# Kernel tuning notes

Measured on AMD Instinct MI355X. Metric: run time of the kernel, lower is better.

The kernel has to match this reference:

```python
import jax, jax.numpy as jnp
import numpy as np

EMBED_DIM = 1024
NUM_HEADS = 16
HEAD_WIDTH = 64  # EMBED_DIM == NUM_HEADS * HEAD_WIDTH
B, L = 2, 1024


def setup_inputs() -> dict:
    key = jax.random.key(0)
    ks = jax.random.split(key, 7)
    s = EMBED_DIM ** -0.5
    return {
        "x": jax.random.normal(ks[0], (B, L, EMBED_DIM), dtype=jnp.float32),
        "bias": jax.random.normal(ks[1], (B, L, L, NUM_HEADS), dtype=jnp.float32),
        # nn.Linear weights are (out_features, in_features)
        "w_proj": jax.random.normal(ks[2], (3 * EMBED_DIM, EMBED_DIM), dtype=jnp.float32) * s,
        "w_o": jax.random.normal(ks[3], (EMBED_DIM, EMBED_DIM), dtype=jnp.float32) * s,
        "b_o": jnp.zeros((EMBED_DIM,), dtype=jnp.float32),
        "w_g": jax.random.normal(ks[4], (EMBED_DIM, EMBED_DIM), dtype=jnp.float32) * s,
        "b_g": jnp.ones((EMBED_DIM,), dtype=jnp.float32),
    }


def reference(x, bias, w_proj, w_o, b_o, w_g, b_g):
    b, l, e = x.shape
    h, hw = NUM_HEADS, HEAD_WIDTH
    # fused QKV projection: (B,L,3E) -> (B,H,L,3*hw), head-major split as in torch
    t = jnp.einsum('ble,fe->blf', x, w_proj)
    t = t.reshape(b, l, h, 3 * hw).transpose(0, 2, 1, 3)  # (B,H,L,3hw)
    q, k, v = jnp.split(t, 3, axis=-1)
    q = q * (hw ** -0.5)
    a = jnp.einsum('bhqc,bhkc->bhqk', q, k)
    a = a + bias.transpose(0, 3, 1, 2)  # bias: (B,Lq,Lk,H) -> (B,H,Lq,Lk)
    a = jax.nn.softmax(a, axis=-1)
    y = jnp.einsum('bhqk,bhkc->bqhc', a, v).reshape(b, l, e)
    g = jax.nn.sigmoid(jnp.einsum('ble,fe->blf', x, w_g) + b_g)
    y = g * y
    y = jnp.einsum('ble,fe->blf', y, w_o) + b_o
    # faithful to original rearrange('... lq lk h -> ... h lq lk') applied to (B,h,lq,lk):
    attn = jnp.transpose(a, (0, 3, 1, 2))  # (B, lk, h, lq)
    return y, attn
```

## Files before the change

kernel.cpp:

```cpp
#include <hip/hip_runtime.h>
#include <hip/hip_bf16.h>
#include <stdint.h>

typedef __attribute__((ext_vector_type(4))) float f32x4;
typedef __attribute__((ext_vector_type(8))) short short8;
typedef __attribute__((ext_vector_type(4))) unsigned short u16x4;
typedef unsigned short us;

#define DEV __device__ __forceinline__
#define MFMA16(a, b, c) __builtin_amdgcn_mfma_f32_16x16x32_bf16(a, b, c, 0, 0, 0)

DEV us f2b(float x) {
  union { float f; uint32_t u; } c; c.f = x;
  uint32_t r = (c.u + 0x7fffu + ((c.u >> 16) & 1u)) >> 16;
  return (us)r;
}
DEV float b2f(us x) {
  union { uint32_t u; float f; } c; c.u = ((uint32_t)x) << 16;
  return c.f;
}

DEV void gload_lds16(const void* g, void* l) {
  __builtin_amdgcn_global_load_lds((const __attribute__((address_space(1))) void*)g,
                                   (__attribute__((address_space(3))) void*)l, 16, 0, 0);
}

__global__ __launch_bounds__(256) void prep_k(
    const float* __restrict__ x, const float* __restrict__ wproj,
    const float* __restrict__ wg, const float* __restrict__ wo,
    us* __restrict__ Xbf, us* __restrict__ Wbf, us* __restrict__ Wobf) {
  int i = blockIdx.x * 256 + threadIdx.x;
  const float* src; us* dst;
  if (i < 524288)               { src = x     + (size_t)i * 4;                  dst = Xbf + (size_t)i * 4; }
  else if (i < 524288 + 786432) { int j = i - 524288;            src = wproj + (size_t)j * 4; dst = Wbf + (size_t)j * 4; }
  else if (i < 524288 + 786432 + 262144) { int j = i - (524288 + 786432); src = wg + (size_t)j * 4; dst = Wbf + 3145728 + (size_t)j * 4; }
  else                          { int j = i - (524288 + 786432 + 262144); src = wo + (size_t)j * 4; dst = Wobf + (size_t)j * 4; }
  f32x4 v = *(const f32x4*)src;
  u16x4 o; o.x = f2b(v.x); o.y = f2b(v.y); o.z = f2b(v.z); o.w = f2b(v.w);
  *(u16x4*)dst = o;
}

DEV void gemm_stage(char* sm, const us* A, const us* Bw,
                    int tileMrow, int tileNrow, int buf, int kt, int lane, int wid) {
  const char* gA = (const char*)A;
  const char* gB = (const char*)Bw;
#pragma unroll
  for (int i = 0; i < 2; ++i) {
    int c = wid * 2 + i;
    int off = c * 1024 + lane * 16;
    int r = off >> 6, cb = off & 63;
    gload_lds16(gA + ((size_t)(tileMrow + r) * 2048) + kt * 64 + cb, sm + buf * 8192 + c * 1024);
    gload_lds16(gB + ((size_t)(tileNrow + r) * 2048) + kt * 64 + cb, sm + 16384 + buf * 8192 + c * 1024);
  }
}

DEV void gemm_main(const us* A, const us* Bw,
                   int tileMrow, int tileNrow, f32x4 acc[4][4], char* sm) {
  int tid = threadIdx.x, lane = tid & 63, wid = tid >> 6;
  int wr = wid >> 1, wc = wid & 1;
  gemm_stage(sm, A, Bw, tileMrow, tileNrow, 0, 0, lane, wid);
  for (int kt = 0; kt < 32; ++kt) {
    __syncthreads();
    if (kt < 31) gemm_stage(sm, A, Bw, tileMrow, tileNrow, (kt + 1) & 1, kt + 1, lane, wid);
    int ab = (kt & 1) * 8192;
    int rb = (lane & 15) * 64 + ((lane >> 4) * 16);
    short8 af[4], bf[4];
#pragma unroll
    for (int mi = 0; mi < 4; ++mi)
      af[mi] = *(const short8*)(sm + ab + (wr * 64 + mi * 16) * 64 + rb);
#pragma unroll
    for (int ni = 0; ni < 4; ++ni)
      bf[ni] = *(const short8*)(sm + 16384 + ab + (wc * 64 + ni * 16) * 64 + rb);
#pragma unroll
    for (int mi = 0; mi < 4; ++mi)
#pragma unroll
      for (int ni = 0; ni < 4; ++ni)
        acc[mi][ni] = MFMA16(af[mi], bf[ni], acc[mi][ni]);
  }
}

__global__ __launch_bounds__(256) void gemm_qkvg_k(
    const us* __restrict__ Xbf, const us* __restrict__ Wbf,
    us* __restrict__ Qb, us* __restrict__ Kb, us* __restrict__ Vt,
    float* __restrict__ G, const float* __restrict__ bg) {
  __shared__ char sm[32768];
  int bid = blockIdx.x;
  int swz = (bid & 7) * 64 + (bid >> 3);
  int tileM = swz >> 5, tileN = swz & 31;
  f32x4 acc[4][4] = {};
  gemm_main(Xbf, Wbf, tileM * 128, tileN * 128, acc, sm);
  int lane = threadIdx.x & 63, wid = threadIdx.x >> 6;
  int wr = wid >> 1, wc = wid & 1;
#pragma unroll
  for (int mi = 0; mi < 4; ++mi)
#pragma unroll
    for (int ni = 0; ni < 4; ++ni)
#pragma unroll
      for (int j = 0; j < 4; ++j) {
        int row = tileM * 128 + wr * 64 + mi * 16 + ((lane >> 4) << 2) + j;
        int col = tileN * 128 + wc * 64 + ni * 16 + (lane & 15);
        float v = acc[mi][ni][j];
        int b = row >> 10, l = row & 1023;
        if (col < 3072) {
          int h = col / 192, r = col - h * 192;
          size_t base = ((size_t)(b * 16 + h) * 1024 + l) * 64;
          if (r < 64)        Qb[base + r] = f2b(v * 0.125f);
          else if (r < 128)  Kb[base + (r - 64)] = f2b(v);
          else               Vt[((size_t)(b * 16 + h) * 64 + (r - 128)) * 1024 + l] = f2b(v);
        } else {
          int e = col - 3072;
          float s = v + bg[e];
          G[(size_t)row * 1024 + e] = 1.f / (1.f + __expf(-s));
        }
      }
}

__global__ __launch_bounds__(512, 4) void qke_k(
    const us* __restrict__ Qb, const us* __restrict__ Kb,
    const float* __restrict__ bias, us* __restrict__ E,
    float* __restrict__ lpart) {
  __shared__ float bt[2][4][8][16][36];
  int tid = threadIdx.x, lane = tid & 63, w = tid >> 6;
  int la = lane & 15, lg = lane >> 4;
  int bid = blockIdx.x;
  int b = (bid & 7) >> 2, kc = bid & 3;
  int hg = (bid >> 3) & 1, qt = bid >> 4;
  int lq0 = qt * 16, lk00 = kc * 256;
  int h = hg * 8 + w, hh = w;

  short8 qf[2];
  {
    size_t bh = (size_t)(b * 16 + h);
#pragma unroll
    for (int ks = 0; ks < 2; ++ks)
      qf[ks] = *(const short8*)(Qb + bh * 65536 + (size_t)(lq0 + la) * 64 + ks * 32 + lg * 8);
  }
  const us* Kh = Kb + (size_t)(b * 16 + h) * 65536;
  const float* bsrc = bias + ((size_t)b << 24) + ((size_t)lq0 << 14) + hg * 8;
  us* Erow = E + (((size_t)(b * 1024 + lq0 + la) * 16 + h) << 10);

  f32x4 vv[8];
#pragma unroll
  for (int i = 0; i < 8; ++i) {
    int f = i * 512 + tid;
    int h4 = f & 1, lk = (f >> 1) & 127, q = f >> 8;
    vv[i] = *(const f32x4*)(bsrc + ((size_t)q << 14) + ((size_t)(lk00 + lk) << 4) + h4 * 4);
  }
#pragma unroll
  for (int i = 0; i < 8; ++i) {
    int f = i * 512 + tid;
    int h4 = f & 1, lk = (f >> 1) & 127, q = f >> 8;
    int c = lk >> 5, slk = lk & 31;
#pragma unroll
    for (int e = 0; e < 4; ++e) {
      int hl = h4 * 4 + e;
      bt[0][c][hl][q][slk ^ (hl << 2)] = vv[i][e];
    }
  }
  __syncthreads();

  float lacc = 0.f;
#pragma unroll
  for (int i = 0; i < 8; ++i) {
    int f = i * 512 + tid;
    int h4 = f & 1, lk = (f >> 1) & 127, q = f >> 8;
    vv[i] = *(const f32x4*)(bsrc + ((size_t)q << 14) + ((size_t)(lk00 + 128 + lk) << 4) + h4 * 4);
  }
#pragma unroll
  for (int fr = 0; fr < 8; ++fr) {
    int c = fr >> 1;
    const us* kr = Kh + (size_t)(lk00 + fr * 16 + la) * 64 + lg * 8;
    short8 kf0 = *(const short8*)kr;
    short8 kf1 = *(const short8*)(kr + 32);
    int lkb = ((fr & 1) * 16 + lg * 4) ^ (hh << 2);
    f32x4 a = *(const f32x4*)&bt[0][c][hh][la][lkb];
    a = MFMA16(kf0, qf[0], a);
    a = MFMA16(kf1, qf[1], a);
    u16x4 ev;
#pragma unroll
    for (int j = 0; j < 4; ++j) {
      float e = __expf(a[j]);
      lacc += e;
      ev[j] = f2b(e);
    }
    *(u16x4*)(Erow + lk00 + fr * 16 + lg * 4) = ev;
  }
#pragma unroll
  for (int i = 0; i < 8; ++i) {
    int f = i * 512 + tid;
    int h4 = f & 1, lk = (f >> 1) & 127, q = f >> 8;
    int c = lk >> 5, slk = lk & 31;
#pragma unroll
    for (int e = 0; e < 4; ++e) {
      int hl = h4 * 4 + e;
      bt[1][c][hl][q][slk ^ (hl << 2)] = vv[i][e];
    }
  }
  __syncthreads();
#pragma unroll
  for (int fr = 0; fr < 8; ++fr) {
    int c = fr >> 1;
    const us* kr = Kh + (size_t)(lk00 + 128 + fr * 16 + la) * 64 + lg * 8;
    short8 kf0 = *(const short8*)kr;
    short8 kf1 = *(const short8*)(kr + 32);
    int lkb = ((fr & 1) * 16 + lg * 4) ^ (hh << 2);
    f32x4 a = *(const f32x4*)&bt[1][c][hh][la][lkb];
    a = MFMA16(kf0, qf[0], a);
    a = MFMA16(kf1, qf[1], a);
    u16x4 ev;
#pragma unroll
    for (int j = 0; j < 4; ++j) {
      float e = __expf(a[j]);
      lacc += e;
      ev[j] = f2b(e);
    }
    *(u16x4*)(Erow + lk00 + 128 + fr * 16 + lg * 4) = ev;
  }
  {
    float s = lacc;
    s += __shfl_xor(s, 16);
    s += __shfl_xor(s, 32);
    if (lg == 0) lpart[kc * 32768 + (b * 16 + h) * 1024 + lq0 + la] = s;
  }
}

__global__ __launch_bounds__(256) void pv_k(
    const us* __restrict__ E, const us* __restrict__ Vt,
    const float* __restrict__ lpart, const float* __restrict__ G,
    float* __restrict__ outa, us* __restrict__ Ybf) {
  __shared__ char sm[49792];
  float* lv = (float*)(sm + 49664);
  int tid = threadIdx.x, lane = tid & 63, w = tid >> 6;
  int la = lane & 15, lg = lane >> 4;
  int bid = blockIdx.x;
  int g = bid >> 8, qt = (bid >> 3) & 31, xx = bid & 7;
  int bh = g * 8 + xx;
  int b = bh >> 4, h = bh & 15;
  int qb = qt * 32;
  if (tid < 32) {
    int r = bh * 1024 + qb + tid;
    float s = lpart[r] + lpart[32768 + r] + lpart[65536 + r] + lpart[98304 + r];
    lv[tid] = 1.f / s;
  }
  __syncthreads();
  char* pb = sm + w * 4096;
  const us* Vh = Vt + (size_t)bh * 65536;
  f32x4 yacc[2][4] = {};
  int lkw = w * 256;

#pragma unroll 1
  for (int cc = 0; cc < 4; ++cc) {
    int lk0 = lkw + cc * 64;
#pragma unroll
    for (int it = 0; it < 4; ++it) {
      int ci = it * 64 + lane;
      int q = ci >> 3, c16 = ci & 7;
      short8 ev = *(const short8*)(E + (((size_t)(b * 1024 + qb + q) * 16 + h) << 10) + lk0 + c16 * 8);
      *(short8*)(pb + q * 128 + ((c16 * 16) ^ ((q & 7) << 4))) = ev;
    }
#pragma unroll
    for (int it = 0; it < 8; ++it) {
      int idx = it * 64 + lane;
      int lkL = idx >> 3, q4 = idx & 7;
      f32x4 ov;
#pragma unroll
      for (int i = 0; i < 4; ++i) {
        int q = q4 * 4 + i;
        us e = *(const us*)(pb + q * 128 + ((2 * lkL) ^ ((q & 7) << 4)));
        ov[i] = b2f(e) * lv[q];
      }
      *(f32x4*)(outa + (((size_t)(b * 1024 + lk0 + lkL) * 16 + h) << 10) + qb + q4 * 4) = ov;
    }
#pragma unroll
    for (int ks = 0; ks < 2; ++ks) {
      short8 pa[2];
#pragma unroll
      for (int qh = 0; qh < 2; ++qh) {
        int row = qh * 16 + la;
        pa[qh] = *(const short8*)(pb + row * 128 + ((ks * 64 + lg * 16) ^ ((row & 7) << 4)));
      }
#pragma unroll
      for (int ni = 0; ni < 4; ++ni) {
        short8 vf = *(const short8*)(Vh + (size_t)(ni * 16 + la) * 1024 + lk0 + ks * 32 + lg * 8);
        yacc[0][ni] = MFMA16(pa[0], vf, yacc[0][ni]);
        yacc[1][ni] = MFMA16(pa[1], vf, yacc[1][ni]);
      }
    }
  }

  float* red = (float*)(sm + 16384);
#pragma unroll
  for (int qh = 0; qh < 2; ++qh)
#pragma unroll
    for (int ni = 0; ni < 4; ++ni)
#pragma unroll
      for (int j = 0; j < 4; ++j) {
        int r = qh * 16 + lg * 4 + j, c = ni * 16 + la;
        red[w * 2080 + r * 65 + c] = yacc[qh][ni][j];
      }
  __syncthreads();
#pragma unroll
  for (int rr = 0; rr < 8; ++rr) {
    int e = rr * 256 + tid;
    int r = e >> 6, c = e & 63;
    float s = red[r * 65 + c] + red[2080 + r * 65 + c] +
              red[4160 + r * 65 + c] + red[6240 + r * 65 + c];
    size_t gi = (((size_t)(b * 1024 + qb + r)) << 10) + h * 64 + c;
    Ybf[gi] = f2b(s * lv[r] * G[gi]);
  }
}

__global__ __launch_bounds__(256) void gemm_out_k(
    const us* __restrict__ Ybf, const us* __restrict__ Wobf,
    const float* __restrict__ bo, float* __restrict__ outy) {
  __shared__ char sm[32768];
  int bid = blockIdx.x;
  int swz = (bid & 7) * 16 + (bid >> 3);
  int tileM = swz >> 3, tileN = swz & 7;
  f32x4 acc[4][4] = {};
  gemm_main(Ybf, Wobf, tileM * 128, tileN * 128, acc, sm);
  int lane = threadIdx.x & 63, wid = threadIdx.x >> 6;
  int wr = wid >> 1, wc = wid & 1;
#pragma unroll
  for (int mi = 0; mi < 4; ++mi)
#pragma unroll
    for (int ni = 0; ni < 4; ++ni)
#pragma unroll
      for (int j = 0; j < 4; ++j) {
        int row = tileM * 128 + wr * 64 + mi * 16 + ((lane >> 4) << 2) + j;
        int col = tileN * 128 + wc * 64 + ni * 16 + (lane & 15);
        outy[(size_t)row * 1024 + col] = acc[mi][ni][j] + bo[col];
      }
}

extern "C" void kernel_launch(void* const* d_in, const int* in_sizes, int n_in,
                              void* d_out, int out_size, void* d_ws, size_t ws_size,
                              hipStream_t stream) {
  const float* x     = (const float*)d_in[0];
  const float* bias  = (const float*)d_in[1];
  const float* wproj = (const float*)d_in[2];
  const float* wo    = (const float*)d_in[3];
  const float* bo    = (const float*)d_in[4];
  const float* wg    = (const float*)d_in[5];
  const float* bg    = (const float*)d_in[6];
  float* outy = (float*)d_out;
  float* outa = outy + 2097152;

  char* ws = (char*)d_ws;
  us*    Xbf  = (us*)(ws);
  us*    Wbf  = (us*)(ws + 4  * 1024 * 1024);
  us*    Wobf = (us*)(ws + 12 * 1024 * 1024);
  us*    Qb   = (us*)(ws + 14 * 1024 * 1024);
  us*    Kb   = (us*)(ws + 18 * 1024 * 1024);
  us*    Vt   = (us*)(ws + 22 * 1024 * 1024);
  float* G    = (float*)(ws + 26 * 1024 * 1024);
  us*    Ybf  = (us*)(ws + 34 * 1024 * 1024);
  float* lpart= (float*)(ws + (size_t)38 * 1024 * 1024);
  us*    E    = (us*)   (ws + (size_t)40 * 1024 * 1024);
  if (ws_size < (size_t)104 * 1024 * 1024) return;

  prep_k<<<dim3(7168), dim3(256), 0, stream>>>(x, wproj, wg, wo, Xbf, Wbf, Wobf);
  gemm_qkvg_k<<<dim3(512), dim3(256), 0, stream>>>(Xbf, Wbf, Qb, Kb, Vt, G, bg);
  qke_k<<<dim3(1024), dim3(512), 0, stream>>>(Qb, Kb, bias, E, lpart);
  pv_k<<<dim3(1024), dim3(256), 0, stream>>>(E, Vt, lpart, G, outa, Ybf);
  gemm_out_k<<<dim3(128), dim3(256), 0, stream>>>(Ybf, Wobf, bo, outy);
}
```

Baseline: 195.1 us.

## Restructure qke kernel to cover all heads per block with 4-stage bias pipeline

Each qke block now covers all 16 heads, with each wave handling two heads, instead of splitting heads across two blocks. Bias reads therefore fetch full 64-byte head rows per key position, giving more contiguous global loads. The key range is processed in four 64-wide chunks with a double-buffered LDS prefetch loop, and the grid is halved. This trades per-block parallelism and occupancy (launch bound min-blocks removed, more registers for two Q fragments) for better bias coalescing and deeper overlap.

```diff
diff --git a/kernel.cpp b/kernel.cpp
--- a/kernel.cpp
+++ b/kernel.cpp
@@ -115,112 +115,108 @@
       }
 }
 
-__global__ __launch_bounds__(512, 4) void qke_k(
+__global__ __launch_bounds__(512) void qke_k(
     const us* __restrict__ Qb, const us* __restrict__ Kb,
     const float* __restrict__ bias, us* __restrict__ E,
     float* __restrict__ lpart) {
-  __shared__ float bt[2][4][8][16][36];
+  __shared__ float bt[2][2][16][16][36];
   int tid = threadIdx.x, lane = tid & 63, w = tid >> 6;
   int la = lane & 15, lg = lane >> 4;
   int bid = blockIdx.x;
   int b = (bid & 7) >> 2, kc = bid & 3;
-  int hg = (bid >> 3) & 1, qt = bid >> 4;
+  int qt = bid >> 3;
   int lq0 = qt * 16, lk00 = kc * 256;
-  int h = hg * 8 + w, hh = w;
-
-  short8 qf[2];
-  {
-    size_t bh = (size_t)(b * 16 + h);
+
+  short8 qf[2][2];
+#pragma unroll
+  for (int s = 0; s < 2; ++s) {
+    size_t bh = (size_t)(b * 16 + w * 2 + s);
 #pragma unroll
     for (int ks = 0; ks < 2; ++ks)
-      qf[ks] = *(const short8*)(Qb + bh * 65536 + (size_t)(lq0 + la) * 64 + ks * 32 + lg * 8);
-  }
-  const us* Kh = Kb + (size_t)(b * 16 + h) * 65536;
-  const float* bsrc = bias + ((size_t)b << 24) + ((size_t)lq0 << 14) + hg * 8;
-  us* Erow = E + (((size_t)(b * 1024 + lq0 + la) * 16 + h) << 10);
+      qf[s][ks] = *(const short8*)(Qb + bh * 65536 + (size_t)(lq0 + la) * 64 + ks * 32 + lg * 8);
+  }
+  const float* bsrc = bias + ((size_t)b << 24) + ((size_t)lq0 << 14);
 
   f32x4 vv[8];
 #pragma unroll
   for (int i = 0; i < 8; ++i) {
     int f = i * 512 + tid;
-    int h4 = f & 1, lk = (f >> 1) & 127, q = f >> 8;
+    int h4 = f & 3, lk = (f >> 2) & 63, q = f >> 8;
     vv[i] = *(const f32x4*)(bsrc + ((size_t)q << 14) + ((size_t)(lk00 + lk) << 4) + h4 * 4);
   }
 #pragma unroll
   for (int i = 0; i < 8; ++i) {
     int f = i * 512 + tid;
-    int h4 = f & 1, lk = (f >> 1) & 127, q = f >> 8;
+    int h4 = f & 3, lk = (f >> 2) & 63, q = f >> 8;
     int c = lk >> 5, slk = lk & 31;
 #pragma unroll
     for (int e = 0; e < 4; ++e) {
-      int hl = h4 * 4 + e;
-      bt[0][c][hl][q][slk ^ (hl << 2)] = vv[i][e];
-    }
-  }
-  __syncthreads();
-
-  float lacc = 0.f;
-#pragma unroll
-  for (int i = 0; i < 8; ++i) {
-    int f = i * 512 + tid;
-    int h4 = f & 1, lk = (f >> 1) & 127, q = f >> 8;
-    vv[i] = *(const f32x4*)(bsrc + ((size_t)q << 14) + ((size_t)(lk00 + 128 + lk) << 4) + h4 * 4);
-  }
-#pragma unroll
-  for (int fr = 0; fr < 8; ++fr) {
-    int c = fr >> 1;
-    const us* kr = Kh + (size_t)(lk00 + fr * 16 + la) * 64 + lg * 8;
-    short8 kf0 = *(const short8*)kr;
-    short8 kf1 = *(const short8*)(kr + 32);
-    int lkb = ((fr & 1) * 16 + lg * 4) ^ (hh << 2);
-    f32x4 a = *(const f32x4*)&bt[0][c][hh][la][lkb];
-    a = MFMA16(kf0, qf[0], a);
-    a = MFMA16(kf1, qf[1], a);
-    u16x4 ev;
-#pragma unroll
-    for (int j = 0; j < 4; ++j) {
-      float e = __expf(a[j]);
-      lacc += e;
-      ev[j] = f2b(e);
-    }
-    *(u16x4*)(Erow + lk00 + fr * 16 + lg * 4) = ev;
-  }
-#pragma unroll
-  for (int i = 0; i < 8; ++i) {
-    int f = i * 512 + tid;
-    int h4 = f & 1, lk = (f >> 1) & 127, q = f >> 8;
-    int c = lk >> 5, slk = lk & 31;
-#pragma unroll
-    for (int e = 0; e < 4; ++e) {
-      int hl = h4 * 4 + e;
-      bt[1][c][hl][q][slk ^ (hl << 2)] = vv[i][e];
-    }
-  }
-  __syncthreads();
-#pragma unroll
-  for (int fr = 0; fr < 8; ++fr) {
-    int c = fr >> 1;
-    const us* kr = Kh + (size_t)(lk00 + 128 + fr * 16 + la) * 64 + lg * 8;
-    short8 kf0 = *(const short8*)kr;
-    short8 kf1 = *(const short8*)(kr + 32);
-    int lkb = ((fr & 1) * 16 + lg * 4) ^ (hh << 2);
-    f32x4 a = *(const f32x4*)&bt[1][c][hh][la][lkb];
-    a = MFMA16(kf0, qf[0], a);
-    a = MFMA16(kf1, qf[1], a);
-    u16x4 ev;
-#pragma unroll
-    for (int j = 0; j < 4; ++j) {
-      float e = __expf(a[j]);
-      lacc += e;
-      ev[j] = f2b(e);
-    }
-    *(u16x4*)(Erow + lk00 + 128 + fr * 16 + lg * 4) = ev;
-  }
-  {
-    float s = lacc;
-    s += __shfl_xor(s, 16);
-    s += __shfl_xor(s, 32);
-    if (lg == 0) lpart[kc * 32768 + (b * 16 + h) * 1024 + lq0 + la] = s;
+      int h = h4 * 4 + e;
+      bt[0][c][h][q][slk ^ ((h & 7) << 2)] = vv[i][e];
+    }
+  }
+
+  float lacc[2] = {0.f, 0.f};
+#pragma unroll 1
+  for (int t = 0; t < 4; ++t) {
+    __syncthreads();
+    if (t < 3) {
+      int lkt = lk00 + (t + 1) * 64;
+#pragma unroll
+      for (int i = 0; i < 8; ++i) {
+        int f = i * 512 + tid;
+        int h4 = f & 3, lk = (f >> 2) & 63, q = f >> 8;
+        vv[i] = *(const f32x4*)(bsrc + ((size_t)q << 14) + ((size_t)(lkt + lk) << 4) + h4 * 4);
+      }
+    }
+    int cb = t & 1;
+    int lkt0 = lk00 + t * 64;
+#pragma unroll
+    for (int s = 0; s < 2; ++s) {
+      int h = w * 2 + s;
+      const us* Kh = Kb + (size_t)(b * 16 + h) * 65536;
+      us* Erow = E + (((size_t)(b * 1024 + lq0 + la) * 16 + h) << 10);
+#pragma unroll
+      for (int fr = 0; fr < 4; ++fr) {
+        const us* kr = Kh + (size_t)(lkt0 + fr * 16 + la) * 64 + lg * 8;
+        short8 kf0 = *(const short8*)kr;
+        short8 kf1 = *(const short8*)(kr + 32);
+        int c = fr >> 1;
+        int lkb = ((fr & 1) * 16 + lg * 4) ^ ((h & 7) << 2);
+        f32x4 a = *(const f32x4*)&bt[cb][c][h][la][lkb];
+        a = MFMA16(kf0, qf[s][0], a);
+        a = MFMA16(kf1, qf[s][1], a);
+        u16x4 ev;
+#pragma unroll
+        for (int j = 0; j < 4; ++j) {
+          float e = __expf(a[j]);
+          lacc[s] += e;
+          ev[j] = f2b(e);
+        }
+        *(u16x4*)(Erow + lkt0 + fr * 16 + lg * 4) = ev;
+      }
+    }
+    if (t < 3) {
+      int nb = (t + 1) & 1;
+#pragma unroll
+      for (int i = 0; i < 8; ++i) {
+        int f = i * 512 + tid;
+        int h4 = f & 3, lk = (f >> 2) & 63, q = f >> 8;
+        int c = lk >> 5, slk = lk & 31;
+#pragma unroll
+        for (int e = 0; e < 4; ++e) {
+          int h = h4 * 4 + e;
+          bt[nb][c][h][q][slk ^ ((h & 7) << 2)] = vv[i][e];
+        }
+      }
+    }
+  }
+#pragma unroll
+  for (int s = 0; s < 2; ++s) {
+    float v = lacc[s];
+    v += __shfl_xor(v, 16);
+    v += __shfl_xor(v, 32);
+    if (lg == 0) lpart[kc * 32768 + (b * 16 + w * 2 + s) * 1024 + lq0 + la] = v;
   }
 }
 
@@ -361,7 +357,7 @@
 
   prep_k<<<dim3(7168), dim3(256), 0, stream>>>(x, wproj, wg, wo, Xbf, Wbf, Wobf);
   gemm_qkvg_k<<<dim3(512), dim3(256), 0, stream>>>(Xbf, Wbf, Qb, Kb, Vt, G, bg);
-  qke_k<<<dim3(1024), dim3(512), 0, stream>>>(Qb, Kb, bias, E, lpart);
+  qke_k<<<dim3(512), dim3(512), 0, stream>>>(Qb, Kb, bias, E, lpart);
   pv_k<<<dim3(1024), dim3(256), 0, stream>>>(E, Vt, lpart, G, outa, Ybf);
   gemm_out_k<<<dim3(128), dim3(256), 0, stream>>>(Ybf, Wobf, bo, outy);
 }
```

New measurement: 199.8 us. 1.02x slower.
